# Kernel tuning notes

Measured on AMD Instinct MI355X. Metric: run time of the kernel, lower is better.

## Reference

```python
import jax, jax.numpy as jnp
import numpy as np

B, S, D, HID, H, VOCAB, DFF = 4, 2048, 512, 512, 8, 32000, 2048
DK = HID // H   # per-head Q/K dim
DV = D // H     # per-head V dim


def sinusoidal_pe(L, d):
    pos = jnp.arange(L, dtype=jnp.float32)[:, None]
    i = jnp.arange(d, dtype=jnp.float32)[None, :]
    ang = pos / jnp.power(jnp.float32(10000.0), i / d)
    return jnp.where(jnp.arange(d)[None, :] % 2 == 0, jnp.sin(ang), jnp.cos(ang))  # [L, d]


def layer_norm(x, gamma, beta, eps=1e-5):
    mu = jnp.mean(x, axis=-1, keepdims=True)
    var = jnp.mean((x - mu) ** 2, axis=-1, keepdims=True)
    return (x - mu) * jax.lax.rsqrt(var + eps) * gamma + beta


def setup_inputs() -> dict:
    key = jax.random.key(0)
    ks = jax.random.split(key, 24)
    n = lambda k, shape, fan: jax.random.normal(k, shape, dtype=jnp.float32) / np.sqrt(fan)
    inp = {
        'x': jax.random.randint(ks[0], (B, S), 0, VOCAB),
        'emb': n(ks[1], (VOCAB, D), D),
        'WfQ': n(ks[2], (D, HID), D), 'bfQ': jnp.zeros((HID,), jnp.float32),
        'WfK': n(ks[3], (D, HID), D), 'bfK': jnp.zeros((HID,), jnp.float32),
        'WfV': n(ks[4], (D, D), D),   'bfV': jnp.zeros((D,), jnp.float32),
        'WQ': n(ks[5], (H, HID, DK), HID), 'bQ': jnp.zeros((H, DK), jnp.float32),
        'WK': n(ks[6], (H, HID, DK), HID), 'bK': jnp.zeros((H, DK), jnp.float32),
        'WV': n(ks[7], (H, D, DV), D),     'bV': jnp.zeros((H, DV), jnp.float32),
        'Wo': n(ks[8], (D, D), D),   'bo': jnp.zeros((D,), jnp.float32),
        'W1': n(ks[9], (D, DFF), D), 'b1': jnp.zeros((DFF,), jnp.float32),
        'W2': n(ks[10], (DFF, D), DFF), 'b2': jnp.zeros((D,), jnp.float32),
        'gamma': jnp.ones((D,), jnp.float32), 'beta': jnp.zeros((D,), jnp.float32),
    }
    return inp


def reference(x, emb, WfQ, bfQ, WfK, bfK, WfV, bfV, WQ, bQ, WK, bK, WV, bV,
              Wo, bo, W1, b1, W2, b2, gamma, beta):
    z = emb[x] + sinusoidal_pe(x.shape[1], D)[None]            # [B,S,D]
    Q = z @ WfQ + bfQ                                           # [B,S,HID]
    K = z @ WfK + bfK
    V = z @ WfV + bfV                                           # [B,S,D]
    # per-head projections (batched equivalent of the per-head Linear loop)
    Qh = jnp.einsum('bsd,hdk->bhsk', Q, WQ) + bQ[None, :, None, :]  # [B,H,S,DK]
    Kh = jnp.einsum('bsd,hdk->bhsk', K, WK) + bK[None, :, None, :]
    Vh = jnp.einsum('bsd,hdv->bhsv', V, WV) + bV[None, :, None, :]  # [B,H,S,DV]
    scores = jnp.einsum('bhqk,bhsk->bhqs', Qh, Kh) / np.sqrt(DK)    # [B,H,S,S]
    attn = jax.nn.softmax(scores, axis=-1)
    heads = jnp.einsum('bhqs,bhsv->bhqv', attn, Vh)                 # [B,H,S,DV]
    concat = heads.transpose(0, 2, 1, 3).reshape(x.shape[0], x.shape[1], D)
    attn_out = concat @ Wo + bo
    a = layer_norm(attn_out + z, gamma, beta)
    ffn = jax.nn.relu(a @ W1 + b1) @ W2 + b2
    out = layer_norm(ffn + a, gamma, beta)   # same (shared) LayerNorm params, as in source
    return jax.nn.relu(out)
```

## Files before the change

kernel.cpp:

```cpp
#include <hip/hip_runtime.h>
#include <math.h>

typedef __bf16 bf16;
typedef __bf16 bf16x8 __attribute__((ext_vector_type(8)));
typedef __bf16 bf16x4 __attribute__((ext_vector_type(4)));
typedef _Float16 f16;
typedef _Float16 f16x8 __attribute__((ext_vector_type(8)));
typedef _Float16 f16x4 __attribute__((ext_vector_type(4)));
typedef _Float16 f16x2 __attribute__((ext_vector_type(2)));
typedef __fp16 h16x2 __attribute__((ext_vector_type(2)));
typedef float f32x4 __attribute__((ext_vector_type(4)));
typedef unsigned int u32;

#define S_LEN 2048
#define QSCALE 0.18033688011112042f

__device__ __forceinline__ void gload_lds16(const void* g, void* l) {
  __builtin_amdgcn_global_load_lds((const __attribute__((address_space(1))) u32*)g,
                                   (__attribute__((address_space(3))) u32*)l, 16, 0, 0);
}

__global__ __launch_bounds__(256) void embed_pe(const int* __restrict__ x,
    const float* __restrict__ emb, float* __restrict__ zf, bf16* __restrict__ zb)
{
  const int row = blockIdx.x;
  const int s = row & (S_LEN - 1);
  const int tok = x[row];
  const float* e = emb + (size_t)tok * 512;
  float* zr = zf + (size_t)row * 512;
  bf16* zbr = zb + (size_t)row * 512;
  for (int i = threadIdx.x; i < 512; i += 256) {
    float invf = __expf((float)i * (-9.210340371976184f / 512.0f));
    float ang = (float)s * invf;
    float pe = (i & 1) ? __cosf(ang) : __sinf(ang);
    float v = e[i] + pe;
    zr[i] = v;
    zbr[i] = (bf16)v;
  }
}

__global__ __launch_bounds__(256) void conv_all(
    const float* __restrict__ WfQ, const float* __restrict__ WfK, const float* __restrict__ WfV,
    const float* __restrict__ WQ, const float* __restrict__ WK, const float* __restrict__ WV,
    const float* __restrict__ Wo, const float* __restrict__ W1, const float* __restrict__ W2,
    bf16* __restrict__ wfqp, bf16* __restrict__ wfkp, bf16* __restrict__ wfvp,
    bf16* __restrict__ wqt, bf16* __restrict__ wkt, bf16* __restrict__ wvt,
    bf16* __restrict__ wot, bf16* __restrict__ w1t, bf16* __restrict__ w2t)
{
  int gid = blockIdx.x * 256 + threadIdx.x;
  int y = blockIdx.y;
  if (y < 3) {
    if (gid >= 262144) return;
    const float* in = y == 0 ? WfQ : (y == 1 ? WfK : WfV);
    bf16* out = y == 0 ? wfqp : (y == 1 ? wfkp : wfvp);
    out[gid] = (bf16)in[gid];
  } else if (y < 6) {
    if (gid >= 262144) return;
    const float* in = y == 3 ? WQ : (y == 4 ? WK : WV);
    bf16* out = y == 3 ? wqt : (y == 4 ? wkt : wvt);
    float scale = y == 3 ? QSCALE : 1.0f;
    int r = gid & 511, t = gid >> 9, c = t & 63, h = t >> 6;
    out[gid] = (bf16)(in[((size_t)(h * 512 + r)) * 64 + c] * scale);
  } else if (y == 6) {
    if (gid >= 262144) return;
    int r = gid & 511, c = gid >> 9;
    wot[gid] = (bf16)Wo[r * 512 + c];
  } else if (y == 7) {
    int r = gid & 511, c = gid >> 9;
    w1t[gid] = (bf16)W1[r * 2048 + c];
  } else {
    int r = gid & 2047, c = gid >> 11;
    w2t[gid] = (bf16)W2[r * 512 + c];
  }
}

__global__ __launch_bounds__(256) void bias_comb(
    const float* __restrict__ bfQ, const float* __restrict__ bfK, const float* __restrict__ bfV,
    const float* __restrict__ WQ, const float* __restrict__ WK, const float* __restrict__ WV,
    const float* __restrict__ bQ, const float* __restrict__ bK, const float* __restrict__ bV,
    float* __restrict__ bc)
{
  int n = blockIdx.x * 4 + (threadIdx.x >> 6);
  int lane = threadIdx.x & 63;
  int z = n >> 9, hk = n & 511, h = hk >> 6, k = hk & 63;
  const float* bf = z == 0 ? bfQ : (z == 1 ? bfK : bfV);
  const float* W  = z == 0 ? WQ  : (z == 1 ? WK  : WV);
  const float* bH = z == 0 ? bQ  : (z == 1 ? bK  : bV);
  float s = 0.f;
  for (int e = lane; e < 512; e += 64)
    s += bf[e] * W[((size_t)h * 512 + e) * 64 + k];
  #pragma unroll
  for (int m = 1; m < 64; m <<= 1) s += __shfl_xor(s, m, 64);
  if (lane == 0) {
    float v = s + bH[h * 64 + k];
    if (z == 0) v *= QSCALE;
    bc[n] = v;
  }
}

__global__ __launch_bounds__(256) void gemm_comb(
    const bf16* __restrict__ wqt, const bf16* __restrict__ wkt, const bf16* __restrict__ wvt,
    const bf16* __restrict__ wfqp, const bf16* __restrict__ wfkp, const bf16* __restrict__ wfvp,
    bf16* __restrict__ wc)
{
  __shared__ bf16 As[128 * 32];
  __shared__ bf16 Bs[64 * 32];
  const int z = blockIdx.z;
  const bf16* A  = z == 0 ? wqt : (z == 1 ? wkt : wvt);
  const bf16* Bt = z == 0 ? wfqp : (z == 1 ? wfkp : wfvp);
  bf16* outb = wc + (size_t)z * 262144;
  const int tid = threadIdx.x;
  const int wave = tid >> 6, lane = tid & 63, quad = lane >> 4, l16 = lane & 15;
  const int row0 = blockIdx.x * 128, col0 = blockIdx.y * 64;
  const int wm = wave >> 1, wn = wave & 1;
  f32x4 acc[4][2] = {};

  for (int kk = 0; kk < 512; kk += 32) {
    __syncthreads();
    #pragma unroll
    for (int r = 0; r < 2; r++) {
      int c = r * 256 + tid;
      gload_lds16(A + (size_t)(row0 + (c >> 2)) * 512 + kk + (c & 3) * 8, As + c * 8);
    }
    gload_lds16(Bt + (size_t)(col0 + (tid >> 2)) * 512 + kk + (tid & 3) * 8, Bs + tid * 8);
    __syncthreads();
    bf16x8 af[4], bfr[2];
    #pragma unroll
    for (int i = 0; i < 4; i++)
      af[i] = *(const bf16x8*)(As + (wm * 64 + i * 16 + l16) * 32 + quad * 8);
    #pragma unroll
    for (int i = 0; i < 2; i++)
      bfr[i] = *(const bf16x8*)(Bs + (wn * 32 + i * 16 + l16) * 32 + quad * 8);
    #pragma unroll
    for (int mt = 0; mt < 4; mt++)
      #pragma unroll
      for (int nt = 0; nt < 2; nt++)
        acc[mt][nt] = __builtin_amdgcn_mfma_f32_16x16x32_bf16(af[mt], bfr[nt], acc[mt][nt], 0, 0, 0);
  }
  #pragma unroll
  for (int nt = 0; nt < 2; nt++) {
    int col = col0 + wn * 32 + nt * 16 + l16;
    #pragma unroll
    for (int mt = 0; mt < 4; mt++) {
      int rowb = row0 + wm * 64 + mt * 16 + quad * 4;
      #pragma unroll
      for (int i = 0; i < 4; i++)
        outb[(size_t)(rowb + i) * 512 + col] = (bf16)acc[mt][nt][i];
    }
  }
}

#define GEMM_CORE(A_, Bt_, K_, KK0_, ITERS_)                                            \
  bf16x8 ar0, ar1, br0, br1;                                                            \
  const int c0 = tid, c1 = 256 + tid;                                                   \
  const size_t aoff0 = (size_t)(row0 + (c0 >> 2)) * (K_) + (c0 & 3) * 8;                \
  const size_t aoff1 = (size_t)(row0 + (c1 >> 2)) * (K_) + (c1 & 3) * 8;                \
  const size_t boff0 = (size_t)(col0 + (c0 >> 2)) * (K_) + (c0 & 3) * 8;                \
  const size_t boff1 = (size_t)(col0 + (c1 >> 2)) * (K_) + (c1 & 3) * 8;                \
  ar0 = *(const bf16x8*)((A_) + aoff0 + (KK0_));                                        \
  ar1 = *(const bf16x8*)((A_) + aoff1 + (KK0_));                                        \
  br0 = *(const bf16x8*)((Bt_) + boff0 + (KK0_));                                       \
  br1 = *(const bf16x8*)((Bt_) + boff1 + (KK0_));                                       \
  for (int it = 0; it < (ITERS_); it++) {                                               \
    bf16* AsB = As[it & 1];                                                             \
    bf16* BsB = Bs[it & 1];                                                             \
    *(bf16x8*)(AsB + c0 * 8) = ar0;                                                     \
    *(bf16x8*)(AsB + c1 * 8) = ar1;                                                     \
    *(bf16x8*)(BsB + c0 * 8) = br0;                                                     \
    *(bf16x8*)(BsB + c1 * 8) = br1;                                                     \
    __syncthreads();                                                                    \
    if (it + 1 < (ITERS_)) {                                                            \
      int kk = (KK0_) + (it + 1) * 32;                                                  \
      ar0 = *(const bf16x8*)((A_) + aoff0 + kk);                                        \
      ar1 = *(const bf16x8*)((A_) + aoff1 + kk);                                        \
      br0 = *(const bf16x8*)((Bt_) + boff0 + kk);                                       \
      br1 = *(const bf16x8*)((Bt_) + boff1 + kk);                                       \
    }                                                                                   \
    bf16x8 af[4], bfr[4];                                                               \
    _Pragma("unroll")                                                                   \
    for (int i = 0; i < 4; i++)                                                         \
      af[i] = *(const bf16x8*)(AsB + (wm * 64 + i * 16 + l16) * 32 + quad * 8);         \
    _Pragma("unroll")                                                                   \
    for (int i = 0; i < 4; i++)                                                         \
      bfr[i] = *(const bf16x8*)(BsB + (wn * 64 + i * 16 + l16) * 32 + quad * 8);        \
    _Pragma("unroll")                                                                   \
    for (int mt = 0; mt < 4; mt++)                                                      \
      _Pragma("unroll")                                                                 \
      for (int nt = 0; nt < 4; nt++)                                                    \
        acc[mt][nt] = __builtin_amdgcn_mfma_f32_16x16x32_bf16(af[mt], bfr[nt], acc[mt][nt], 0, 0, 0); \
  }

__global__ __launch_bounds__(256) void gemm_bt(
    const bf16* __restrict__ A, const bf16* __restrict__ Bt,
    const float* __restrict__ bias, bf16* __restrict__ outb,
    int M, int N, int K, int relu)
{
  __shared__ bf16 As[2][4096];
  __shared__ bf16 Bs[2][4096];
  const int tid = threadIdx.x;
  const int wave = tid >> 6, lane = tid & 63, quad = lane >> 4, l16 = lane & 15;
  const int row0 = blockIdx.x * 128, col0 = blockIdx.y * 128;
  const int wm = wave >> 1, wn = wave & 1;
  f32x4 acc[4][4] = {};
  GEMM_CORE(A, Bt, K, 0, K / 32)

  #pragma unroll
  for (int nt = 0; nt < 4; nt++) {
    int col = col0 + wn * 64 + nt * 16 + l16;
    float bv = bias[col];
    #pragma unroll
    for (int mt = 0; mt < 4; mt++) {
      int rowb = row0 + wm * 64 + mt * 16 + quad * 4;
      #pragma unroll
      for (int i = 0; i < 4; i++) {
        float v = acc[mt][nt][i] + bv;
        if (relu) v = fmaxf(v, 0.f);
        outb[(size_t)(rowb + i) * N + col] = (bf16)v;
      }
    }
  }
}

__global__ __launch_bounds__(256) void gemm_qkv(
    const bf16* __restrict__ A, const bf16* __restrict__ Bt,
    const float* __restrict__ bias, f16* __restrict__ qk, f16* __restrict__ Vt)
{
  __shared__ bf16 As[2][4096];
  __shared__ bf16 Bs[2][4096];
  const int tid = threadIdx.x;
  const int wave = tid >> 6, lane = tid & 63, quad = lane >> 4, l16 = lane & 15;
  const int row0 = blockIdx.x * 128, col0 = blockIdx.y * 128;
  const int wm = wave >> 1, wn = wave & 1;
  f32x4 acc[4][4] = {};
  GEMM_CORE(A, Bt, 512, 0, 16)

  #pragma unroll
  for (int nt = 0; nt < 4; nt++) {
    int col = col0 + wn * 64 + nt * 16 + l16;
    float bv = bias[col];
    if (col < 1024) {
      #pragma unroll
      for (int mt = 0; mt < 4; mt++) {
        int rowb = row0 + wm * 64 + mt * 16 + quad * 4;
        #pragma unroll
        for (int i = 0; i < 4; i++)
          qk[(size_t)(rowb + i) * 1024 + col] = (f16)(acc[mt][nt][i] + bv);
      }
    } else {
      int h = (col - 1024) >> 6, dv = col & 63;
      #pragma unroll
      for (int mt = 0; mt < 4; mt++) {
        int rowb = row0 + wm * 64 + mt * 16 + quad * 4;
        int b = rowb >> 11, s = rowb & 2047;
        f16x4 vv;
        #pragma unroll
        for (int i = 0; i < 4; i++) vv[i] = (f16)(acc[mt][nt][i] + bv);
        *(f16x4*)(Vt + ((size_t)((b * 8 + h) * 64 + dv)) * 2048 + s) = vv;
      }
    }
  }
}

__global__ __launch_bounds__(256) void gemm_part(
    const bf16* __restrict__ A, const bf16* __restrict__ Bt,
    bf16* __restrict__ Pa, bf16* __restrict__ Pb, int N, int K, int Kh)
{
  __shared__ bf16 As[2][4096];
  __shared__ bf16 Bs[2][4096];
  const int tid = threadIdx.x;
  const int wave = tid >> 6, lane = tid & 63, quad = lane >> 4, l16 = lane & 15;
  const int row0 = blockIdx.x * 128, col0 = blockIdx.y * 128;
  const int wm = wave >> 1, wn = wave & 1;
  const int kk0 = blockIdx.z * Kh;
  bf16* P = blockIdx.z ? Pb : Pa;
  f32x4 acc[4][4] = {};
  GEMM_CORE(A, Bt, K, kk0, Kh / 32)

  #pragma unroll
  for (int nt = 0; nt < 4; nt++) {
    int col = col0 + wn * 64 + nt * 16 + l16;
    #pragma unroll
    for (int mt = 0; mt < 4; mt++) {
      int rowb = row0 + wm * 64 + mt * 16 + quad * 4;
      #pragma unroll
      for (int i = 0; i < 4; i++)
        P[(size_t)(rowb + i) * N + col] = (bf16)acc[mt][nt][i];
    }
  }
}

__global__ __launch_bounds__(256) void flash_attn(
    const f16* __restrict__ qk, const f16* __restrict__ Vt,
    bf16* __restrict__ Op, float* __restrict__ Rp)
{
  __shared__ f16 Ks[2][4096];
  __shared__ f16 Vs[2][4096];
  const int bh = blockIdx.y, b = bh >> 3, h = bh & 7;
  const int q0 = blockIdx.x * 128;
  const int half = blockIdx.z;
  const int tid = threadIdx.x;
  const int wave = tid >> 6, lane = tid & 63, quad = lane >> 4, l16 = lane & 15;

  const f16* Qb = qk + ((size_t)b * S_LEN) * 1024 + h * 64;
  const f16* Kb = Qb + 512;
  const f16* Vtb = Vt + ((size_t)bh * 64) * 2048;
  const int key0 = half * 1024;

  f16x8 qf[2][2];
  #pragma unroll
  for (int f = 0; f < 2; f++) {
    int qrow = q0 + wave * 32 + f * 16 + l16;
    #pragma unroll
    for (int kh = 0; kh < 2; kh++)
      qf[f][kh] = *(const f16x8*)(Qb + (size_t)qrow * 1024 + kh * 32 + quad * 8);
  }

  f32x4 O[2][4] = {};
  f32x4 Osum[2] = {};
  const f16x4 onesA = {(f16)1.f, (f16)1.f, (f16)1.f, (f16)1.f};
  const int swz = l16 & 7;

  f16x8 kreg[2], vreg[2];
  const int srow = tid >> 3, soff = tid & 7;
  const int srow1 = srow + 32;

  {
    int kb = key0;
    kreg[0] = *(const f16x8*)(Kb + (size_t)(kb + srow) * 1024 + soff * 8);
    vreg[0] = *(const f16x8*)(Vtb + (size_t)srow * 2048 + kb + soff * 8);
    kreg[1] = *(const f16x8*)(Kb + (size_t)(kb + srow1) * 1024 + soff * 8);
    vreg[1] = *(const f16x8*)(Vtb + (size_t)srow1 * 2048 + kb + soff * 8);
  }

  for (int c = 0; c < 16; c++) {
    f16* KsB = Ks[c & 1];
    f16* VsB = Vs[c & 1];
    *(f16x8*)(KsB + srow * 64 + ((soff ^ (srow & 7)) * 8)) = kreg[0];
    *(f16x8*)(VsB + srow * 64 + ((soff ^ (srow & 7)) * 8)) = vreg[0];
    *(f16x8*)(KsB + srow1 * 64 + ((soff ^ (srow1 & 7)) * 8)) = kreg[1];
    *(f16x8*)(VsB + srow1 * 64 + ((soff ^ (srow1 & 7)) * 8)) = vreg[1];
    __syncthreads();
    if (c < 15) {
      int kb = key0 + (c + 1) * 64;
      kreg[0] = *(const f16x8*)(Kb + (size_t)(kb + srow) * 1024 + soff * 8);
      vreg[0] = *(const f16x8*)(Vtb + (size_t)srow * 2048 + kb + soff * 8);
      kreg[1] = *(const f16x8*)(Kb + (size_t)(kb + srow1) * 1024 + soff * 8);
      vreg[1] = *(const f16x8*)(Vtb + (size_t)srow1 * 2048 + kb + soff * 8);
    }

    #pragma unroll
    for (int nt = 0; nt < 4; nt++) {
      const f16* kp = KsB + (nt * 16 + l16) * 64;
      f16x8 kf0 = *(const f16x8*)(kp + ((quad ^ swz) * 8));
      f16x8 kf1 = *(const f16x8*)(kp + (((4 + quad) ^ swz) * 8));
      f16x4 pf[2];
      #pragma unroll
      for (int f = 0; f < 2; f++) {
        f32x4 a = {};
        a = __builtin_amdgcn_mfma_f32_16x16x32_f16(kf0, qf[f][0], a, 0, 0, 0);
        a = __builtin_amdgcn_mfma_f32_16x16x32_f16(kf1, qf[f][1], a, 0, 0, 0);
        float e0 = exp2f(a[0]);
        float e1 = exp2f(a[1]);
        float e2 = exp2f(a[2]);
        float e3 = exp2f(a[3]);
        h16x2 lo = __builtin_amdgcn_cvt_pkrtz(e0, e1);
        h16x2 hi = __builtin_amdgcn_cvt_pkrtz(e2, e3);
        f16x2 lo2 = __builtin_bit_cast(f16x2, lo);
        f16x2 hi2 = __builtin_bit_cast(f16x2, hi);
        pf[f] = __builtin_shufflevector(lo2, hi2, 0, 1, 2, 3);
        Osum[f] = __builtin_amdgcn_mfma_f32_16x16x16f16(onesA, pf[f], Osum[f], 0, 0, 0);
      }
      int vchunk = nt * 2 + (quad >> 1);
      #pragma unroll
      for (int mt = 0; mt < 4; mt++) {
        const f16* vp = VsB + (mt * 16 + l16) * 64 + ((vchunk ^ swz) * 8) + (quad & 1) * 4;
        f16x4 vf = *(const f16x4*)vp;
        #pragma unroll
        for (int f = 0; f < 2; f++)
          O[f][mt] = __builtin_amdgcn_mfma_f32_16x16x16f16(vf, pf[f], O[f][mt], 0, 0, 0);
      }
    }
    __syncthreads();
  }

  #pragma unroll
  for (int f = 0; f < 2; f++) {
    bf16* ob = (f == 0 ? (bf16*)&Ks[0][0] : (bf16*)&Vs[0][0]) + wave * 1152;
    #pragma unroll
    for (int mt = 0; mt < 4; mt++)
      #pragma unroll
      for (int i = 0; i < 4; i++)
        ob[l16 * 72 + mt * 16 + quad * 4 + i] = (bf16)O[f][mt][i];
  }
  asm volatile("s_waitcnt lgkmcnt(0)" ::: "memory");
  const size_t obase = (size_t)(half * 32 + bh) * 2048;
  #pragma unroll
  for (int f = 0; f < 2; f++) {
    bf16* ob = (f == 0 ? (bf16*)&Ks[0][0] : (bf16*)&Vs[0][0]) + wave * 1152;
    int row = lane >> 2, dvb = (lane & 3) * 16;
    bf16x8 o0 = *(const bf16x8*)(ob + row * 72 + dvb);
    bf16x8 o1 = *(const bf16x8*)(ob + row * 72 + dvb + 8);
    size_t g = (obase + q0 + wave * 32 + f * 16 + row) * 64 + dvb;
    *(bf16x8*)(Op + g) = o0;
    *(bf16x8*)(Op + g + 8) = o1;
    if (quad == f)
      Rp[obase + q0 + wave * 32 + f * 16 + l16] = Osum[f][0];
  }
}

__global__ __launch_bounds__(256) void attn_merge(const bf16* __restrict__ Op,
    const float* __restrict__ Rp, bf16* __restrict__ concat)
{
  int t = blockIdx.x * 256 + threadIdx.x;
  int dv4 = t & 15, s = (t >> 4) & 2047, bh = t >> 15;
  int rb = bh * 2048 + s;
  float r = Rp[rb] + Rp[65536 + rb];
  float inv = 1.f / r;
  size_t ia = ((size_t)bh * 2048 + s) * 64 + dv4 * 4;
  bf16x4 a = *(const bf16x4*)(Op + ia);
  bf16x4 c = *(const bf16x4*)(Op + 4194304ull + ia);
  bf16x4 o;
  #pragma unroll
  for (int i = 0; i < 4; i++) o[i] = (bf16)(((float)a[i] + (float)c[i]) * inv);
  int b = bh >> 3, h = bh & 7;
  *(bf16x4*)(concat + ((size_t)(b * 2048 + s)) * 512 + h * 64 + dv4 * 4) = o;
}

__global__ __launch_bounds__(256) void ln_merge(const bf16* __restrict__ Pa,
    const bf16* __restrict__ Pb, const float* __restrict__ badd,
    const float* __restrict__ resid, const float* __restrict__ gamma,
    const float* __restrict__ beta, float* __restrict__ outf,
    bf16* __restrict__ outb, int relu)
{
  const int row = blockIdx.x * 4 + (threadIdx.x >> 6);
  const int lane = threadIdx.x & 63;
  const size_t base = (size_t)row * 512;
  const int e0 = lane * 8;
  bf16x8 pa = *(const bf16x8*)(Pa + base + e0);
  bf16x8 pb = *(const bf16x8*)(Pb + base + e0);
  float4 R0 = *(const float4*)(resid + base + e0);
  float4 R1 = *(const float4*)(resid + base + e0 + 4);
  float4 C0 = *(const float4*)(badd + e0);
  float4 C1 = *(const float4*)(badd + e0 + 4);
  float v[8];
  v[0] = (float)pa[0] + (float)pb[0] + R0.x + C0.x;
  v[1] = (float)pa[1] + (float)pb[1] + R0.y + C0.y;
  v[2] = (float)pa[2] + (float)pb[2] + R0.z + C0.z;
  v[3] = (float)pa[3] + (float)pb[3] + R0.w + C0.w;
  v[4] = (float)pa[4] + (float)pb[4] + R1.x + C1.x;
  v[5] = (float)pa[5] + (float)pb[5] + R1.y + C1.y;
  v[6] = (float)pa[6] + (float)pb[6] + R1.z + C1.z;
  v[7] = (float)pa[7] + (float)pb[7] + R1.w + C1.w;
  float s = 0.f;
  #pragma unroll
  for (int i = 0; i < 8; i++) s += v[i];
  #pragma unroll
  for (int m = 1; m < 64; m <<= 1) s += __shfl_xor(s, m, 64);
  float mu = s * (1.f / 512.f);
  float d[8], q = 0.f;
  #pragma unroll
  for (int i = 0; i < 8; i++) { d[i] = v[i] - mu; q += d[i] * d[i]; }
  #pragma unroll
  for (int m = 1; m < 64; m <<= 1) q += __shfl_xor(q, m, 64);
  float rs = rsqrtf(q * (1.f / 512.f) + 1e-5f);
  float4 g0 = *(const float4*)(gamma + e0);
  float4 g1 = *(const float4*)(gamma + e0 + 4);
  float4 b0 = *(const float4*)(beta + e0);
  float4 b1 = *(const float4*)(beta + e0 + 4);
  float y[8];
  y[0] = d[0] * rs * g0.x + b0.x; y[1] = d[1] * rs * g0.y + b0.y;
  y[2] = d[2] * rs * g0.z + b0.z; y[3] = d[3] * rs * g0.w + b0.w;
  y[4] = d[4] * rs * g1.x + b1.x; y[5] = d[5] * rs * g1.y + b1.y;
  y[6] = d[6] * rs * g1.z + b1.z; y[7] = d[7] * rs * g1.w + b1.w;
  if (relu) {
    #pragma unroll
    for (int i = 0; i < 8; i++) y[i] = fmaxf(y[i], 0.f);
  }
  float4 o0 = {y[0], y[1], y[2], y[3]}, o1 = {y[4], y[5], y[6], y[7]};
  *(float4*)(outf + base + e0) = o0;
  *(float4*)(outf + base + e0 + 4) = o1;
  if (outb) {
    bf16x8 ob;
    #pragma unroll
    for (int i = 0; i < 8; i++) ob[i] = (bf16)y[i];
    *(bf16x8*)(outb + base + e0) = ob;
  }
}

extern "C" void kernel_launch(void* const* d_in, const int* in_sizes, int n_in,
                              void* d_out, int out_size, void* d_ws, size_t ws_size,
                              hipStream_t stream)
{
  const int*   x    = (const int*)  d_in[0];
  const float* emb  = (const float*)d_in[1];
  const float* WfQ  = (const float*)d_in[2];
  const float* bfQv = (const float*)d_in[3];
  const float* WfK  = (const float*)d_in[4];
  const float* bfKv = (const float*)d_in[5];
  const float* WfV  = (const float*)d_in[6];
  const float* bfVv = (const float*)d_in[7];
  const float* WQ   = (const float*)d_in[8];
  const float* bQ   = (const float*)d_in[9];
  const float* WK   = (const float*)d_in[10];
  const float* bK   = (const float*)d_in[11];
  const float* WV   = (const float*)d_in[12];
  const float* bV   = (const float*)d_in[13];
  const float* Wo   = (const float*)d_in[14];
  const float* bo   = (const float*)d_in[15];
  const float* W1   = (const float*)d_in[16];
  const float* b1   = (const float*)d_in[17];
  const float* W2   = (const float*)d_in[18];
  const float* b2   = (const float*)d_in[19];
  const float* gamma= (const float*)d_in[20];
  const float* beta = (const float*)d_in[21];
  float* out = (float*)d_out;

  char* ws = (char*)d_ws;
  const size_t MB = 1024ull * 1024;
  float* zf   = (float*)(ws);
  bf16*  bz   = (bf16*) (ws + 16 * MB);
  f16*   qkh  = (f16*)  (ws + 24 * MB);
  f16*   Vt   = (f16*)  (ws + 40 * MB);
  bf16*  Op   = (bf16*) (ws + 48 * MB);
  float* Rp   = (float*)(ws + 80 * MB);
  bf16*  concat = (bf16*)(ws + 82 * MB);
  bf16*  PaW  = (bf16*) (ws + 48 * MB);
  bf16*  PbW  = (bf16*) (ws + 56 * MB);
  bf16*  ffn1 = (bf16*) (ws + 24 * MB);
  bf16*  Pa2  = (bf16*) (ws + 56 * MB);
  bf16*  Pb2  = (bf16*) (ws + 64 * MB);
  char* wp = ws + 90 * MB;
  bf16* wfqp = (bf16*)(wp);
  bf16* wfkp = (bf16*)(wp + 512 * 1024);
  bf16* wfvp = (bf16*)(wp + 1024 * 1024);
  bf16* wqt  = (bf16*)(wp + 1536 * 1024);
  bf16* wkt  = (bf16*)(wp + 2048 * 1024);
  bf16* wvt  = (bf16*)(wp + 2560 * 1024);
  bf16* wc   = (bf16*)(wp + 3072 * 1024);
  bf16* wot  = (bf16*)(wp + 4608 * 1024);
  bf16* w1t  = (bf16*)(wp + 5120 * 1024);
  bf16* w2t  = (bf16*)(wp + 7168 * 1024);
  float* bc  = (float*)(wp + 9216 * 1024);

  conv_all<<<dim3(4096, 9), 256, 0, stream>>>(WfQ, WfK, WfV, WQ, WK, WV, Wo, W1, W2,
                                              wfqp, wfkp, wfvp, wqt, wkt, wvt, wot, w1t, w2t);
  bias_comb<<<384, 256, 0, stream>>>(bfQv, bfKv, bfVv, WQ, WK, WV, bQ, bK, bV, bc);
  gemm_comb<<<dim3(4, 8, 3), 256, 0, stream>>>(wqt, wkt, wvt, wfqp, wfkp, wfvp, wc);

  embed_pe<<<8192, 256, 0, stream>>>(x, emb, zf, bz);

  gemm_qkv<<<dim3(64, 12), 256, 0, stream>>>(bz, wc, bc, qkh, Vt);
  flash_attn<<<dim3(16, 32, 2), 256, 0, stream>>>(qkh, Vt, Op, Rp);
  attn_merge<<<4096, 256, 0, stream>>>(Op, Rp, concat);

  gemm_part<<<dim3(64, 4, 2), 256, 0, stream>>>(concat, wot, PaW, PbW, 512, 512, 256);
  ln_merge<<<2048, 256, 0, stream>>>(PaW, PbW, bo, zf, gamma, beta, zf, bz, 0);
  gemm_bt<<<dim3(64, 16), 256, 0, stream>>>(bz, w1t, b1, ffn1, 8192, 2048, 512, 1);
  gemm_part<<<dim3(64, 4, 2), 256, 0, stream>>>(ffn1, w2t, Pa2, Pb2, 512, 2048, 1024);
  ln_merge<<<2048, 256, 0, stream>>>(Pa2, Pb2, b2, zf, gamma, beta, out, nullptr, 1);
}
```

Before: 358.5 us.

## Split attention keys into quarters and keep the residual stream in bf16

The flash-attention grid now splits the key range into four 512-key chunks instead of two 1024-key halves. This doubles the block count and halves the serial loop per block, and the merge kernel combines four partial outputs and row sums. The fp32 copy of the embedding/residual is removed: embed_pe writes only bf16, and both LayerNorm merges read the bf16 residual, with the first one writing its result in place. This cuts global memory traffic but lowers residual precision and adds partial-output traffic in the attention merge.

After: 348.2 us. 2.9% less time.

```diff
diff --git a/kernel.cpp b/kernel.cpp
--- a/kernel.cpp
+++ b/kernel.cpp
@@ -21,21 +21,18 @@
 }
 
 __global__ __launch_bounds__(256) void embed_pe(const int* __restrict__ x,
-    const float* __restrict__ emb, float* __restrict__ zf, bf16* __restrict__ zb)
+    const float* __restrict__ emb, bf16* __restrict__ zb)
 {
   const int row = blockIdx.x;
   const int s = row & (S_LEN - 1);
   const int tok = x[row];
   const float* e = emb + (size_t)tok * 512;
-  float* zr = zf + (size_t)row * 512;
   bf16* zbr = zb + (size_t)row * 512;
   for (int i = threadIdx.x; i < 512; i += 256) {
     float invf = __expf((float)i * (-9.210340371976184f / 512.0f));
     float ang = (float)s * invf;
     float pe = (i & 1) ? __cosf(ang) : __sinf(ang);
-    float v = e[i] + pe;
-    zr[i] = v;
-    zbr[i] = (bf16)v;
+    zbr[i] = (bf16)(e[i] + pe);
   }
 }
 
@@ -297,14 +294,14 @@
   __shared__ f16 Vs[2][4096];
   const int bh = blockIdx.y, b = bh >> 3, h = bh & 7;
   const int q0 = blockIdx.x * 128;
-  const int half = blockIdx.z;
+  const int quarter = blockIdx.z;
   const int tid = threadIdx.x;
   const int wave = tid >> 6, lane = tid & 63, quad = lane >> 4, l16 = lane & 15;
 
   const f16* Qb = qk + ((size_t)b * S_LEN) * 1024 + h * 64;
   const f16* Kb = Qb + 512;
   const f16* Vtb = Vt + ((size_t)bh * 64) * 2048;
-  const int key0 = half * 1024;
+  const int key0 = quarter * 512;
 
   f16x8 qf[2][2];
   #pragma unroll
@@ -332,7 +329,7 @@
     vreg[1] = *(const f16x8*)(Vtb + (size_t)srow1 * 2048 + kb + soff * 8);
   }
 
-  for (int c = 0; c < 16; c++) {
+  for (int c = 0; c < 8; c++) {
     f16* KsB = Ks[c & 1];
     f16* VsB = Vs[c & 1];
     *(f16x8*)(KsB + srow * 64 + ((soff ^ (srow & 7)) * 8)) = kreg[0];
@@ -340,7 +337,7 @@
     *(f16x8*)(KsB + srow1 * 64 + ((soff ^ (srow1 & 7)) * 8)) = kreg[1];
     *(f16x8*)(VsB + srow1 * 64 + ((soff ^ (srow1 & 7)) * 8)) = vreg[1];
     __syncthreads();
-    if (c < 15) {
+    if (c < 7) {
       int kb = key0 + (c + 1) * 64;
       kreg[0] = *(const f16x8*)(Kb + (size_t)(kb + srow) * 1024 + soff * 8);
       vreg[0] = *(const f16x8*)(Vtb + (size_t)srow * 2048 + kb + soff * 8);
@@ -393,7 +390,7 @@
         ob[l16 * 72 + mt * 16 + quad * 4 + i] = (bf16)O[f][mt][i];
   }
   asm volatile("s_waitcnt lgkmcnt(0)" ::: "memory");
-  const size_t obase = (size_t)(half * 32 + bh) * 2048;
+  const size_t obase = (size_t)(quarter * 32 + bh) * 2048;
   #pragma unroll
   for (int f = 0; f < 2; f++) {
     bf16* ob = (f == 0 ? (bf16*)&Ks[0][0] : (bf16*)&Vs[0][0]) + wave * 1152;
@@ -414,21 +411,24 @@
   int t = blockIdx.x * 256 + threadIdx.x;
   int dv4 = t & 15, s = (t >> 4) & 2047, bh = t >> 15;
   int rb = bh * 2048 + s;
-  float r = Rp[rb] + Rp[65536 + rb];
+  float r = (Rp[rb] + Rp[65536 + rb]) + (Rp[131072 + rb] + Rp[196608 + rb]);
   float inv = 1.f / r;
   size_t ia = ((size_t)bh * 2048 + s) * 64 + dv4 * 4;
-  bf16x4 a = *(const bf16x4*)(Op + ia);
-  bf16x4 c = *(const bf16x4*)(Op + 4194304ull + ia);
+  bf16x4 p0 = *(const bf16x4*)(Op + ia);
+  bf16x4 p1 = *(const bf16x4*)(Op + 4194304ull + ia);
+  bf16x4 p2 = *(const bf16x4*)(Op + 8388608ull + ia);
+  bf16x4 p3 = *(const bf16x4*)(Op + 12582912ull + ia);
   bf16x4 o;
   #pragma unroll
-  for (int i = 0; i < 4; i++) o[i] = (bf16)(((float)a[i] + (float)c[i]) * inv);
+  for (int i = 0; i < 4; i++)
+    o[i] = (bf16)((((float)p0[i] + (float)p1[i]) + ((float)p2[i] + (float)p3[i])) * inv);
   int b = bh >> 3, h = bh & 7;
   *(bf16x4*)(concat + ((size_t)(b * 2048 + s)) * 512 + h * 64 + dv4 * 4) = o;
 }
 
 __global__ __launch_bounds__(256) void ln_merge(const bf16* __restrict__ Pa,
     const bf16* __restrict__ Pb, const float* __restrict__ badd,
-    const float* __restrict__ resid, const float* __restrict__ gamma,
+    const bf16* __restrict__ resid, const float* __restrict__ gamma,
     const float* __restrict__ beta, float* __restrict__ outf,
     bf16* __restrict__ outb, int relu)
 {
@@ -438,19 +438,18 @@
   const int e0 = lane * 8;
   bf16x8 pa = *(const bf16x8*)(Pa + base + e0);
   bf16x8 pb = *(const bf16x8*)(Pb + base + e0);
-  float4 R0 = *(const float4*)(resid + base + e0);
-  float4 R1 = *(const float4*)(resid + base + e0 + 4);
+  bf16x8 rr = *(const bf16x8*)(resid + base + e0);
   float4 C0 = *(const float4*)(badd + e0);
   float4 C1 = *(const float4*)(badd + e0 + 4);
   float v[8];
-  v[0] = (float)pa[0] + (float)pb[0] + R0.x + C0.x;
-  v[1] = (float)pa[1] + (float)pb[1] + R0.y + C0.y;
-  v[2] = (float)pa[2] + (float)pb[2] + R0.z + C0.z;
-  v[3] = (float)pa[3] + (float)pb[3] + R0.w + C0.w;
-  v[4] = (float)pa[4] + (float)pb[4] + R1.x + C1.x;
-  v[5] = (float)pa[5] + (float)pb[5] + R1.y + C1.y;
-  v[6] = (float)pa[6] + (float)pb[6] + R1.z + C1.z;
-  v[7] = (float)pa[7] + (float)pb[7] + R1.w + C1.w;
+  v[0] = (float)pa[0] + (float)pb[0] + (float)rr[0] + C0.x;
+  v[1] = (float)pa[1] + (float)pb[1] + (float)rr[1] + C0.y;
+  v[2] = (float)pa[2] + (float)pb[2] + (float)rr[2] + C0.z;
+  v[3] = (float)pa[3] + (float)pb[3] + (float)rr[3] + C0.w;
+  v[4] = (float)pa[4] + (float)pb[4] + (float)rr[4] + C1.x;
+  v[5] = (float)pa[5] + (float)pb[5] + (float)rr[5] + C1.y;
+  v[6] = (float)pa[6] + (float)pb[6] + (float)rr[6] + C1.z;
+  v[7] = (float)pa[7] + (float)pb[7] + (float)rr[7] + C1.w;
   float s = 0.f;
   #pragma unroll
   for (int i = 0; i < 8; i++) s += v[i];
@@ -476,9 +475,11 @@
     #pragma unroll
     for (int i = 0; i < 8; i++) y[i] = fmaxf(y[i], 0.f);
   }
-  float4 o0 = {y[0], y[1], y[2], y[3]}, o1 = {y[4], y[5], y[6], y[7]};
-  *(float4*)(outf + base + e0) = o0;
-  *(float4*)(outf + base + e0 + 4) = o1;
+  if (outf) {
+    float4 o0 = {y[0], y[1], y[2], y[3]}, o1 = {y[4], y[5], y[6], y[7]};
+    *(float4*)(outf + base + e0) = o0;
+    *(float4*)(outf + base + e0 + 4) = o1;
+  }
   if (outb) {
     bf16x8 ob;
     #pragma unroll
@@ -517,19 +518,18 @@
 
   char* ws = (char*)d_ws;
   const size_t MB = 1024ull * 1024;
-  float* zf   = (float*)(ws);
-  bf16*  bz   = (bf16*) (ws + 16 * MB);
-  f16*   qkh  = (f16*)  (ws + 24 * MB);
-  f16*   Vt   = (f16*)  (ws + 40 * MB);
-  bf16*  Op   = (bf16*) (ws + 48 * MB);
-  float* Rp   = (float*)(ws + 80 * MB);
-  bf16*  concat = (bf16*)(ws + 82 * MB);
-  bf16*  PaW  = (bf16*) (ws + 48 * MB);
-  bf16*  PbW  = (bf16*) (ws + 56 * MB);
-  bf16*  ffn1 = (bf16*) (ws + 24 * MB);
-  bf16*  Pa2  = (bf16*) (ws + 56 * MB);
-  bf16*  Pb2  = (bf16*) (ws + 64 * MB);
-  char* wp = ws + 90 * MB;
+  bf16*  bz   = (bf16*) (ws);
+  f16*   qkh  = (f16*)  (ws + 8 * MB);
+  f16*   Vt   = (f16*)  (ws + 24 * MB);
+  bf16*  Op   = (bf16*) (ws + 32 * MB);
+  float* Rp   = (float*)(ws + 64 * MB);
+  bf16*  concat = (bf16*)(ws + 66 * MB);
+  bf16*  PaW  = (bf16*) (ws + 32 * MB);
+  bf16*  PbW  = (bf16*) (ws + 40 * MB);
+  bf16*  ffn1 = (bf16*) (ws + 8 * MB);
+  bf16*  Pa2  = (bf16*) (ws + 40 * MB);
+  bf16*  Pb2  = (bf16*) (ws + 48 * MB);
+  char* wp = ws + 74 * MB;
   bf16* wfqp = (bf16*)(wp);
   bf16* wfkp = (bf16*)(wp + 512 * 1024);
   bf16* wfvp = (bf16*)(wp + 1024 * 1024);
@@ -547,15 +547,15 @@
   bias_comb<<<384, 256, 0, stream>>>(bfQv, bfKv, bfVv, WQ, WK, WV, bQ, bK, bV, bc);
   gemm_comb<<<dim3(4, 8, 3), 256, 0, stream>>>(wqt, wkt, wvt, wfqp, wfkp, wfvp, wc);
 
-  embed_pe<<<8192, 256, 0, stream>>>(x, emb, zf, bz);
+  embed_pe<<<8192, 256, 0, stream>>>(x, emb, bz);
 
   gemm_qkv<<<dim3(64, 12), 256, 0, stream>>>(bz, wc, bc, qkh, Vt);
-  flash_attn<<<dim3(16, 32, 2), 256, 0, stream>>>(qkh, Vt, Op, Rp);
+  flash_attn<<<dim3(16, 32, 4), 256, 0, stream>>>(qkh, Vt, Op, Rp);
   attn_merge<<<4096, 256, 0, stream>>>(Op, Rp, concat);
 
   gemm_part<<<dim3(64, 4, 2), 256, 0, stream>>>(concat, wot, PaW, PbW, 512, 512, 256);
-  ln_merge<<<2048, 256, 0, stream>>>(PaW, PbW, bo, zf, gamma, beta, zf, bz, 0);
+  ln_merge<<<2048, 256, 0, stream>>>(PaW, PbW, bo, bz, gamma, beta, nullptr, bz, 0);
   gemm_bt<<<dim3(64, 16), 256, 0, stream>>>(bz, w1t, b1, ffn1, 8192, 2048, 512, 1);
   gemm_part<<<dim3(64, 4, 2), 256, 0, stream>>>(ffn1, w2t, Pa2, Pb2, 512, 2048, 1024);
-  ln_merge<<<2048, 256, 0, stream>>>(Pa2, Pb2, b2, zf, gamma, beta, out, nullptr, 1);
-}
+  ln_merge<<<2048, 256, 0, stream>>>(Pa2, Pb2, b2, bz, gamma, beta, out, nullptr, 1);
+}
```
